# Kernel tuning notes

Measured on AMD Instinct MI355X. Metric: run time of the kernel, lower is better.

Reference implementation:

```python
import jax, jax.numpy as jnp
import numpy as np

C_IN = 32
C_OUT = 32


def setup_inputs() -> dict:
    key = jax.random.key(0)
    k1, k2, k3 = jax.random.split(key, 3)
    B, N, P_DIM = 32, 4096, 64
    X = jax.random.normal(k1, (B, N, C_IN), dtype=jnp.float32)
    P = jax.random.normal(k2, (B, N, P_DIM), dtype=jnp.float32)
    # glorot-ish scale for the hypernetwork Dense kernel (p_dim -> c_in*c_out)
    scale = (2.0 / (P_DIM + C_IN * C_OUT)) ** 0.5
    Wk = jax.random.normal(k3, (P_DIM, C_IN * C_OUT), dtype=jnp.float32) * scale
    return {"X": X, "P": P, "Wk": Wk}


def reference(X, P, Wk):
    B, N, c_in = X.shape
    # hypernetwork: per-position weight generation  [B,N,p] @ [p, c_in*c_out]
    A = jnp.einsum('bnp,pq->bnq', P, Wk)
    W = A.reshape(B, N, c_in, C_OUT)          # [B,N,c_in,c_out]
    W = jax.nn.relu(W)                        # sigma(W)
    # batched per-position GEMV: y_bno = sum_i X_bni * W_bnio
    out = jnp.einsum('bni,bnio->bno', X, W)   # [B,N,c_out]
    return out
```

## Files before the change

### kernel.cpp

```cpp
#include <hip/hip_runtime.h>

#define CI 32
#define CO 32
#define PD 64
#define QDIM 1024
#define M_TOTAL (32*4096)
#define WG_THREADS 512
#define NBLK 512
#define TILE_M 64
#define NT 8

typedef float  f32x2  __attribute__((ext_vector_type(2)));
typedef float  f32x4  __attribute__((ext_vector_type(4)));
typedef __bf16 bf16x4 __attribute__((ext_vector_type(4)));
typedef __bf16 bf16x8 __attribute__((ext_vector_type(8)));

#define XL_STRIDE 72
#define OL_STRIDE 20

__global__ __launch_bounds__(256)
void wk_transpose_kernel(const float* __restrict__ Wk, __bf16* __restrict__ wsT)
{
    __shared__ float tile[64][68];
    const int q0 = blockIdx.x * 64;
    const int t  = threadIdx.x;
#pragma unroll
    for (int rr = 0; rr < 4; ++rr) {
        const int k = (t >> 4) + rr * 16;
        const int cc = (t & 15) * 4;
        f32x4 v = *(const f32x4*)(Wk + (size_t)k * QDIM + q0 + cc);
        tile[k][cc] = v[0]; tile[k][cc+1] = v[1]; tile[k][cc+2] = v[2]; tile[k][cc+3] = v[3];
    }
    __syncthreads();
    const int qq = t >> 2, ks = (t & 3) * 16;
    bf16x8 o0, o1;
#pragma unroll
    for (int j = 0; j < 8; ++j) { o0[j] = (__bf16)tile[ks + j][qq]; o1[j] = (__bf16)tile[ks + 8 + j][qq]; }
    *(bf16x8*)(wsT + (size_t)(q0 + qq) * PD + ks)     = o0;
    *(bf16x8*)(wsT + (size_t)(q0 + qq) * PD + ks + 8) = o1;
}

__global__ __launch_bounds__(WG_THREADS, 4)
void cond_dense_kernel(const float* __restrict__ Xg, const float* __restrict__ Pg,
                       const __bf16* __restrict__ wsT, float* __restrict__ outg)
{
    __shared__ __bf16 Pl[TILE_M * PD];
    __shared__ float  Xl[CI * XL_STRIDE];
    __shared__ float  Ol[TILE_M * OL_STRIDE];

    const int tid = threadIdx.x;
    const int l   = tid & 63;
    const int w   = tid >> 6;
    const int h   = l >> 4;
    const int c   = l & 15;
    const int di  = c >> 1;
    const int dq  = c & 1;

    const int col0  = (blockIdx.x >> 8) * 16;
    const int tbase = (blockIdx.x & 255) * NT;

    bf16x8 bfrag[4][2];
#pragma unroll
    for (int t = 0; t < 4; ++t) {
        const int q = (8*t + di) * CO + col0 + 2*w + dq;
#pragma unroll
        for (int s = 0; s < 2; ++s)
            bfrag[t][s] = *(const bf16x8*)(wsT + (size_t)q * PD + s*32 + h*8);
    }
#pragma unroll
    for (int t = 0; t < 4; ++t)
        asm volatile("" : "+v"(bfrag[t][0]), "+v"(bfrag[t][1]));

    const int prow = tid >> 4;
    const int pg   = (tid & 15) >> 1;
    const int ph8  = (tid & 1) * 8;
    const int pcol = (tid & 15) * 4;
    const int xrow = tid >> 3;
    const int xcol = (tid & 7) * 4;

    f32x4 pr0, pr1, xr;
    auto load_stage = [&](int tile) {
        const float* Pb = Pg + (size_t)tile * TILE_M * PD;
        const float* Xb = Xg + (size_t)tile * TILE_M * CI;
        pr0 = *(const f32x4*)(Pb + prow * PD + pcol);
        pr1 = *(const f32x4*)(Pb + (prow + 32) * PD + pcol);
        xr  = *(const f32x4*)(Xb + xrow * CI + xcol);
    };
    auto pl_ptr = [&](int row) -> __bf16* {
        return (__bf16*)((char*)Pl + row * 128 + (((pg ^ (row & 7)) << 4) | ph8));
    };
    auto write_lds = [&]() {
        bf16x4 a0, a1;
#pragma unroll
        for (int j = 0; j < 4; ++j) { a0[j] = (__bf16)pr0[j]; a1[j] = (__bf16)pr1[j]; }
        *(bf16x4*)pl_ptr(prow)      = a0;
        *(bf16x4*)pl_ptr(prow + 32) = a1;
#pragma unroll
        for (int j = 0; j < 4; ++j) Xl[(xcol + j) * XL_STRIDE + xrow] = xr[j];
    };

    load_stage(tbase);
    write_lds();
    __syncthreads();

    for (int it = 0; it < NT; ++it) {
        const int tile = tbase + it;
        if (it + 1 < NT) load_stage(tile + 1);

#pragma unroll
        for (int sub = 0; sub < 4; ++sub) {
            const int m0 = sub * 16;
            const char* prow_b = (const char*)Pl + (m0 + c) * 128;
            bf16x8 af0 = *(const bf16x8*)(prow_b + (((h    ) ^ (c & 7)) << 4));
            bf16x8 af1 = *(const bf16x8*)(prow_b + (((h + 4) ^ (c & 7)) << 4));

            f32x4 acc[4] = {};
#pragma unroll
            for (int t = 0; t < 4; ++t) {
                acc[t] = __builtin_amdgcn_mfma_f32_16x16x32_bf16(af0, bfrag[t][0], acc[t], 0, 0, 0);
                acc[t] = __builtin_amdgcn_mfma_f32_16x16x32_bf16(af1, bfrag[t][1], acc[t], 0, 0, 0);
            }
            f32x4 part = {};
#pragma unroll
            for (int t = 0; t < 4; ++t) {
                const int i = 8*t + di;
                f32x4 xv = *(const f32x4*)(&Xl[i * XL_STRIDE + m0 + h*4]);
#pragma unroll
                for (int r = 0; r < 4; ++r)
                    part[r] += fmaxf(acc[t][r], 0.0f) * xv[r];
            }
            const bool b0 = (di & 1) != 0, b1 = (di & 2) != 0;
            const float lo_k = b0 ? part[1] : part[0];
            const float lo_s = b0 ? part[0] : part[1];
            const float hi_k = b0 ? part[3] : part[2];
            const float hi_s = b0 ? part[2] : part[3];
            const float u = lo_k + __shfl_xor(lo_s, 2);
            const float v = hi_k + __shfl_xor(hi_s, 2);
            const float keep = b1 ? v : u;
            const float send = b1 ? u : v;
            const float hf  = keep + __shfl_xor(send, 4);
            const float res = hf + __shfl_xor(hf, 8);
            if ((di & 4) == 0)
                Ol[(m0 + h*4 + (di & 3)) * OL_STRIDE + 2*w + dq] = res;
        }

        __syncthreads();

        {
            float* outp = outg + (size_t)tile * TILE_M * CO + col0;
            const int row = tid >> 3, cc = (tid & 7) * 2;
            f32x2 o = *(const f32x2*)(&Ol[row * OL_STRIDE + cc]);
            *(f32x2*)(outp + row * CO + cc) = o;
        }

        if (it + 1 < NT) {
            write_lds();
            __syncthreads();
        }
    }
}

extern "C" void kernel_launch(void* const* d_in, const int* in_sizes, int n_in,
                              void* d_out, int out_size, void* d_ws, size_t ws_size,
                              hipStream_t stream)
{
    const float* X  = (const float*)d_in[0];
    const float* P  = (const float*)d_in[1];
    const float* Wk = (const float*)d_in[2];
    float* out = (float*)d_out;
    __bf16* wsT = (__bf16*)d_ws;

    wk_transpose_kernel<<<dim3(QDIM / 64), dim3(256), 0, stream>>>(Wk, wsT);
    cond_dense_kernel<<<dim3(NBLK), dim3(WG_THREADS), 0, stream>>>(X, P, wsT, out);
}
```

Baseline: 39.99 us.

## Drop Wk transpose kernel and double-buffer LDS to halve barriers

```diff
diff --git a/kernel.cpp b/kernel.cpp
--- a/kernel.cpp
+++ b/kernel.cpp
@@ -18,35 +18,13 @@
 #define XL_STRIDE 72
 #define OL_STRIDE 20
 
-__global__ __launch_bounds__(256)
-void wk_transpose_kernel(const float* __restrict__ Wk, __bf16* __restrict__ wsT)
-{
-    __shared__ float tile[64][68];
-    const int q0 = blockIdx.x * 64;
-    const int t  = threadIdx.x;
-#pragma unroll
-    for (int rr = 0; rr < 4; ++rr) {
-        const int k = (t >> 4) + rr * 16;
-        const int cc = (t & 15) * 4;
-        f32x4 v = *(const f32x4*)(Wk + (size_t)k * QDIM + q0 + cc);
-        tile[k][cc] = v[0]; tile[k][cc+1] = v[1]; tile[k][cc+2] = v[2]; tile[k][cc+3] = v[3];
-    }
-    __syncthreads();
-    const int qq = t >> 2, ks = (t & 3) * 16;
-    bf16x8 o0, o1;
-#pragma unroll
-    for (int j = 0; j < 8; ++j) { o0[j] = (__bf16)tile[ks + j][qq]; o1[j] = (__bf16)tile[ks + 8 + j][qq]; }
-    *(bf16x8*)(wsT + (size_t)(q0 + qq) * PD + ks)     = o0;
-    *(bf16x8*)(wsT + (size_t)(q0 + qq) * PD + ks + 8) = o1;
-}
-
 __global__ __launch_bounds__(WG_THREADS, 4)
 void cond_dense_kernel(const float* __restrict__ Xg, const float* __restrict__ Pg,
-                       const __bf16* __restrict__ wsT, float* __restrict__ outg)
+                       const float* __restrict__ Wk, float* __restrict__ outg)
 {
-    __shared__ __bf16 Pl[TILE_M * PD];
-    __shared__ float  Xl[CI * XL_STRIDE];
-    __shared__ float  Ol[TILE_M * OL_STRIDE];
+    __shared__ __bf16 Pl[2][TILE_M * PD];
+    __shared__ float  Xl[2][CI * XL_STRIDE];
+    __shared__ float  Ol[2][TILE_M * OL_STRIDE];
 
     const int tid = threadIdx.x;
     const int l   = tid & 63;
@@ -64,8 +42,13 @@
     for (int t = 0; t < 4; ++t) {
         const int q = (8*t + di) * CO + col0 + 2*w + dq;
 #pragma unroll
-        for (int s = 0; s < 2; ++s)
-            bfrag[t][s] = *(const bf16x8*)(wsT + (size_t)q * PD + s*32 + h*8);
+        for (int s = 0; s < 2; ++s) {
+            bf16x8 f;
+#pragma unroll
+            for (int j = 0; j < 8; ++j)
+                f[j] = (__bf16)Wk[(size_t)(s*32 + h*8 + j) * QDIM + q];
+            bfrag[t][s] = f;
+        }
     }
 #pragma unroll
     for (int t = 0; t < 4; ++t)
@@ -86,31 +69,41 @@
         pr1 = *(const f32x4*)(Pb + (prow + 32) * PD + pcol);
         xr  = *(const f32x4*)(Xb + xrow * CI + xcol);
     };
-    auto pl_ptr = [&](int row) -> __bf16* {
-        return (__bf16*)((char*)Pl + row * 128 + (((pg ^ (row & 7)) << 4) | ph8));
+    auto pl_ptr = [&](int b, int row) -> __bf16* {
+        return (__bf16*)((char*)Pl[b] + row * 128 + (((pg ^ (row & 7)) << 4) | ph8));
     };
-    auto write_lds = [&]() {
+    auto write_lds = [&](int b) {
         bf16x4 a0, a1;
 #pragma unroll
         for (int j = 0; j < 4; ++j) { a0[j] = (__bf16)pr0[j]; a1[j] = (__bf16)pr1[j]; }
-        *(bf16x4*)pl_ptr(prow)      = a0;
-        *(bf16x4*)pl_ptr(prow + 32) = a1;
+        *(bf16x4*)pl_ptr(b, prow)      = a0;
+        *(bf16x4*)pl_ptr(b, prow + 32) = a1;
 #pragma unroll
-        for (int j = 0; j < 4; ++j) Xl[(xcol + j) * XL_STRIDE + xrow] = xr[j];
+        for (int j = 0; j < 4; ++j) Xl[b][(xcol + j) * XL_STRIDE + xrow] = xr[j];
     };
 
     load_stage(tbase);
-    write_lds();
+    write_lds(0);
     __syncthreads();
+
+    const int srow = tid >> 3, scc = (tid & 7) * 2;
 
     for (int it = 0; it < NT; ++it) {
         const int tile = tbase + it;
+        const int b    = it & 1;
+
         if (it + 1 < NT) load_stage(tile + 1);
+
+        if (it > 0) {
+            float* outp = outg + (size_t)(tile - 1) * TILE_M * CO + col0;
+            f32x2 o = *(const f32x2*)(&Ol[b ^ 1][srow * OL_STRIDE + scc]);
+            *(f32x2*)(outp + srow * CO + scc) = o;
+        }
 
 #pragma unroll
         for (int sub = 0; sub < 4; ++sub) {
             const int m0 = sub * 16;
-            const char* prow_b = (const char*)Pl + (m0 + c) * 128;
+            const char* prow_b = (const char*)Pl[b] + (m0 + c) * 128;
             bf16x8 af0 = *(const bf16x8*)(prow_b + (((h    ) ^ (c & 7)) << 4));
             bf16x8 af1 = *(const bf16x8*)(prow_b + (((h + 4) ^ (c & 7)) << 4));
 
@@ -124,7 +117,7 @@
 #pragma unroll
             for (int t = 0; t < 4; ++t) {
                 const int i = 8*t + di;
-                f32x4 xv = *(const f32x4*)(&Xl[i * XL_STRIDE + m0 + h*4]);
+                f32x4 xv = *(const f32x4*)(&Xl[b][i * XL_STRIDE + m0 + h*4]);
 #pragma unroll
                 for (int r = 0; r < 4; ++r)
                     part[r] += fmaxf(acc[t][r], 0.0f) * xv[r];
@@ -141,22 +134,18 @@
             const float hf  = keep + __shfl_xor(send, 4);
             const float res = hf + __shfl_xor(hf, 8);
             if ((di & 4) == 0)
-                Ol[(m0 + h*4 + (di & 3)) * OL_STRIDE + 2*w + dq] = res;
+                Ol[b][(m0 + h*4 + (di & 3)) * OL_STRIDE + 2*w + dq] = res;
         }
 
+        if (it + 1 < NT) write_lds(b ^ 1);
+
         __syncthreads();
+    }
 
-        {
-            float* outp = outg + (size_t)tile * TILE_M * CO + col0;
-            const int row = tid >> 3, cc = (tid & 7) * 2;
-            f32x2 o = *(const f32x2*)(&Ol[row * OL_STRIDE + cc]);
-            *(f32x2*)(outp + row * CO + cc) = o;
-        }
-
-        if (it + 1 < NT) {
-            write_lds();
-            __syncthreads();
-        }
+    {
+        float* outp = outg + (size_t)(tbase + NT - 1) * TILE_M * CO + col0;
+        f32x2 o = *(const f32x2*)(&Ol[(NT - 1) & 1][srow * OL_STRIDE + scc]);
+        *(f32x2*)(outp + srow * CO + scc) = o;
     }
 }
 
@@ -168,8 +157,5 @@
     const float* P  = (const float*)d_in[1];
     const float* Wk = (const float*)d_in[2];
     float* out = (float*)d_out;
-    __bf16* wsT = (__bf16*)d_ws;
-
-    wk_transpose_kernel<<<dim3(QDIM / 64), dim3(256), 0, stream>>>(Wk, wsT);
-    cond_dense_kernel<<<dim3(NBLK), dim3(WG_THREADS), 0, stream>>>(X, P, wsT, out);
+    cond_dense_kernel<<<dim3(NBLK), dim3(WG_THREADS), 0, stream>>>(X, P, Wk, out);
 }
```

After: 63.62 us. 1.59x slower.
